# Kernel optimization log

Measured on AMD Instinct MI355X. Metric: run time of the kernel, lower is better.

## Reference

```python
import jax, jax.numpy as jnp
import numpy as np

NUM_HEADS = 12
HEAD_DIM = 64  # qkv_dim // num_heads = 768 // 12


def setup_inputs() -> dict:
    key = jax.random.key(0)
    ks = jax.random.split(key, 5)
    B, S, Dm = 4, 2048, 768
    x = jax.random.normal(ks[0], (B, S, Dm), dtype=jnp.float32)
    q_mask = jnp.ones((B, S), dtype=jnp.float32)
    sc = 1.0 / np.sqrt(Dm)
    Wq = jax.random.normal(ks[1], (Dm, Dm), dtype=jnp.float32) * sc
    Wk = jax.random.normal(ks[2], (Dm, Dm), dtype=jnp.float32) * sc
    Wv = jax.random.normal(ks[3], (Dm, Dm), dtype=jnp.float32) * sc
    Wo = jax.random.normal(ks[4], (Dm, Dm), dtype=jnp.float32) * sc
    return {"x": x, "q_mask": q_mask, "Wq": Wq, "Wk": Wk, "Wv": Wv, "Wo": Wo}


def _split_heads(t):
    # [b, s, qkv] -> [b, h, s, d]
    b, s, _ = t.shape
    return t.reshape(b, s, NUM_HEADS, HEAD_DIM).transpose(0, 2, 1, 3)


def reference(x, q_mask, Wq, Wk, Wv, Wo):
    # TAttention.forward with k=v=None -> self-attention, k_mask = q_mask.
    q = _split_heads(x @ Wq) * (1.0 / jnp.sqrt(jnp.asarray(HEAD_DIM, x.dtype)))
    k = _split_heads(x @ Wk)
    v = _split_heads(x @ Wv)
    logits_raw = jnp.einsum('bhqd,bhkd->bhqk', q, k)
    # additive mask: mask = outer(q_mask, k_mask) broadcast over heads
    mask = jnp.einsum('bq,bk->bqk', q_mask, q_mask)[:, None]  # [b,1,q,k]
    logits = logits_raw + (-100000.0) * (1.0 - mask)
    att = jax.nn.softmax(logits, axis=-1)  # dropout_rate=0 -> identity
    out = jnp.einsum('bhqk,bhkd->bhqd', att, v)
    b, h, s, d = out.shape
    out = out.transpose(0, 2, 1, 3).reshape(b, s, h * d)
    out = out @ Wo
    return (out, logits_raw)
```

## Files before the change

### kernel.cpp

```cpp
#include <hip/hip_runtime.h>

typedef _Float16 f16;
typedef __attribute__((ext_vector_type(4))) _Float16 f16x4;
typedef __attribute__((ext_vector_type(8))) _Float16 f16x8;
typedef __attribute__((ext_vector_type(4))) float f32x4;

#define NB 4
#define SS 2048
#define DM 768
#define NH 12
#define HDIM 64
#define NBH 48
#define MROWS 8192

#define XH_OFF   0ull
#define WT_OFF   12582912ull
#define QH_OFF   17301504ull
#define KH_OFF   29884416ull
#define VH_OFF   42467328ull
#define VT_OFF   55050240ull
#define AO_OFF   67633152ull

__device__ __forceinline__ void async_copy16(const void* g, void* l) {
  __builtin_amdgcn_global_load_lds((const __attribute__((address_space(1))) void*)g,
                                   (__attribute__((address_space(3))) void*)l, 16, 0, 0);
}

__global__ void k_cvt_x(const float* __restrict__ x, f16* __restrict__ xh, int n4) {
  int i = blockIdx.x * 256 + threadIdx.x;
  if (i >= n4) return;
  float4 v = ((const float4*)x)[i];
  f16x4 o;
  o.x = (f16)v.x; o.y = (f16)v.y; o.z = (f16)v.z; o.w = (f16)v.w;
  ((f16x4*)xh)[i] = o;
}

__global__ void k_wt(const float* __restrict__ Wq, const float* __restrict__ Wk,
                     const float* __restrict__ Wv, const float* __restrict__ Wo,
                     f16* __restrict__ wt) {
  __shared__ float t[32][33];
  const int w = blockIdx.z;
  const float* W = (w == 0) ? Wq : (w == 1) ? Wk : (w == 2) ? Wv : Wo;
  const int bx = blockIdx.x * 32, by = blockIdx.y * 32;
  const int tx = threadIdx.x, ty = threadIdx.y;
  t[ty][tx] = W[(size_t)(by + ty) * DM + bx + tx];
  __syncthreads();
  wt[(size_t)w * DM * DM + (size_t)(bx + ty) * DM + by + tx] = (f16)t[tx][ty];
}

template<int MODE>
__global__ __launch_bounds__(256) void k_gemm(const f16* __restrict__ A,
                                              const f16* __restrict__ Wt,
                                              float* __restrict__ outF,
                                              f16* __restrict__ Qh,
                                              f16* __restrict__ Kh,
                                              f16* __restrict__ Vh) {
  __shared__ f16 Al[128 * 32];
  __shared__ f16 Bl[128 * 32];
  const int tid = threadIdx.x, lane = tid & 63, wid = tid >> 6;
  const int mt = blockIdx.x;
  int w, ntile;
  if (MODE == 0) { w = blockIdx.y / 6; ntile = blockIdx.y % 6; }
  else           { w = 3;              ntile = blockIdx.y; }
  const f16* Wb = Wt + (size_t)w * DM * DM;

  f32x4 acc[4][4] = {};
  const int wr = (wid >> 1) * 64, wc = (wid & 1) * 64;

  const int r0 = tid >> 2, c8 = (tid & 3) * 8;
  const f16* As0 = A  + (size_t)(mt * 128 + r0) * DM + c8;
  const f16* As1 = A  + (size_t)(mt * 128 + r0 + 64) * DM + c8;
  const f16* Bs0 = Wb + (size_t)(ntile * 128 + r0) * DM + c8;
  const f16* Bs1 = Wb + (size_t)(ntile * 128 + r0 + 64) * DM + c8;
  f16* Ald0 = &Al[wid * 512];          f16* Ald1 = &Al[2048 + wid * 512];
  f16* Bld0 = &Bl[wid * 512];          f16* Bld1 = &Bl[2048 + wid * 512];

  for (int k0 = 0; k0 < DM; k0 += 32) {
    __syncthreads();
    async_copy16(As0 + k0, Ald0);
    async_copy16(As1 + k0, Ald1);
    async_copy16(Bs0 + k0, Bld0);
    async_copy16(Bs1 + k0, Bld1);
    __syncthreads();
    f16x8 af[4], bfr[4];
#pragma unroll
    for (int r = 0; r < 4; ++r)
      af[r] = *(const f16x8*)&Al[(wr + r * 16 + (lane & 15)) * 32 + (lane >> 4) * 8];
#pragma unroll
    for (int c = 0; c < 4; ++c)
      bfr[c] = *(const f16x8*)&Bl[(wc + c * 16 + (lane & 15)) * 32 + (lane >> 4) * 8];
#pragma unroll
    for (int r = 0; r < 4; ++r)
#pragma unroll
      for (int c = 0; c < 4; ++c)
        acc[r][c] = __builtin_amdgcn_mfma_f32_16x16x32_f16(af[r], bfr[c], acc[r][c], 0, 0, 0);
  }

#pragma unroll
  for (int r = 0; r < 4; ++r)
#pragma unroll
    for (int c = 0; c < 4; ++c)
#pragma unroll
      for (int i = 0; i < 4; ++i) {
        const int gm = mt * 128 + wr + r * 16 + (lane >> 4) * 4 + i;
        const int gn = ntile * 128 + wc + c * 16 + (lane & 15);
        const float v = acc[r][c][i];
        if (MODE == 1) {
          outF[(size_t)gm * DM + gn] = v;
        } else {
          const int b = gm >> 11, s = gm & 2047;
          const int h = gn >> 6, d = gn & 63;
          const size_t idx = ((size_t)(b * NH + h) * SS + s) * HDIM + d;
          if (w == 0)      Qh[idx] = (f16)(v * 0.125f);
          else if (w == 1) Kh[idx] = (f16)v;
          else             Vh[idx] = (f16)v;
        }
      }
}

__global__ void k_vt(const f16* __restrict__ Vh, f16* __restrict__ Vt) {
  const int lane = threadIdx.x & 63, wid = threadIdx.x >> 6;
  const int s = blockIdx.x * 64 + lane;
  const int bh = blockIdx.y;
#pragma unroll
  for (int p = 0; p < 2; ++p) {
    const int d0 = wid * 16 + p * 8;
    f16x8 v = *(const f16x8*)&Vh[((size_t)bh * SS + s) * HDIM + d0];
#pragma unroll
    for (int q = 0; q < 8; ++q)
      Vt[((size_t)bh * HDIM + d0 + q) * SS + s] = v[q];
  }
}

__global__ __launch_bounds__(256) void k_attn(const f16* __restrict__ Qh,
                                              const f16* __restrict__ Kh,
                                              const f16* __restrict__ Vt,
                                              const float* __restrict__ qm,
                                              float* __restrict__ logits,
                                              f16* __restrict__ AO) {
  __shared__ f16 Kl[64 * 64];
  __shared__ f16 Vl[64 * 64];
  __shared__ f16 Pl[4][16 * 72];
  const int tid = threadIdx.x, lane = tid & 63, wid = tid >> 6;
  const int qt = blockIdx.x, bh = blockIdx.y;
  const int b = bh / NH, h = bh - b * NH;
  const int q0 = qt * 128 + wid * 32;

  f16x8 qf[2][2];
#pragma unroll
  for (int rt = 0; rt < 2; ++rt)
#pragma unroll
    for (int ks = 0; ks < 2; ++ks)
      qf[rt][ks] = *(const f16x8*)&Qh[((size_t)bh * SS + q0 + rt * 16 + (lane & 15)) * HDIM +
                                      ks * 32 + (lane >> 4) * 8];

  float qmq[2][4];
#pragma unroll
  for (int rt = 0; rt < 2; ++rt)
#pragma unroll
    for (int i = 0; i < 4; ++i)
      qmq[rt][i] = qm[b * SS + q0 + rt * 16 + (lane >> 4) * 4 + i];

  float mrun[2][4], lrun[2][4];
#pragma unroll
  for (int rt = 0; rt < 2; ++rt)
#pragma unroll
    for (int i = 0; i < 4; ++i) { mrun[rt][i] = -3.0e38f; lrun[rt][i] = 0.f; }
  f32x4 o[2][4] = {};

  float* const logbase = logits + (size_t)bh * SS * SS;
  const char* const Kbase = (const char*)Kh + (size_t)bh * SS * HDIM * 2;
  const char* const Vbase = (const char*)Vt + (size_t)bh * HDIM * SS * 2;
  const int r0s = tid >> 3;
  const int wb0 = (tid & 7) * 16;

  for (int c = 0; c < 32; ++c) {
    __syncthreads();
#pragma unroll
    for (int j = 0; j < 2; ++j) {
      const int r = r0s + j * 32;
      const int swb = wb0 ^ ((r & 7) << 4);
      async_copy16(Kbase + (size_t)(c * 64 + r) * 128 + swb,
                   (char*)Kl + wid * 1024 + j * 4096);
      async_copy16(Vbase + (size_t)r * 4096 + c * 128 + swb,
                   (char*)Vl + wid * 1024 + j * 4096);
    }
    __syncthreads();

    f16x8 kf[4][2], vf[4][2];
#pragma unroll
    for (int t = 0; t < 4; ++t)
#pragma unroll
      for (int ks = 0; ks < 2; ++ks) {
        const int row = t * 16 + (lane & 15);
        const int byt = row * 128 + ((ks * 64 + (lane >> 4) * 16) ^ ((row & 7) << 4));
        kf[t][ks] = *(const f16x8*)((const char*)Kl + byt);
        vf[t][ks] = *(const f16x8*)((const char*)Vl + byt);
      }

    f32x4 sacc[2][4];
#pragma unroll
    for (int rt = 0; rt < 2; ++rt)
#pragma unroll
      for (int ct = 0; ct < 4; ++ct) {
        f32x4 z = {};
        z = __builtin_amdgcn_mfma_f32_16x16x32_f16(qf[rt][0], kf[ct][0], z, 0, 0, 0);
        sacc[rt][ct] = __builtin_amdgcn_mfma_f32_16x16x32_f16(qf[rt][1], kf[ct][1], z, 0, 0, 0);
      }

#pragma unroll
    for (int rt = 0; rt < 2; ++rt)
#pragma unroll
      for (int ct = 0; ct < 4; ++ct)
#pragma unroll
        for (int i = 0; i < 4; ++i) {
          const int gq = q0 + rt * 16 + (lane >> 4) * 4 + i;
          const int gk = c * 64 + ct * 16 + (lane & 15);
          logbase[(size_t)gq * SS + gk] = sacc[rt][ct][i];
        }

    float qmk[4];
#pragma unroll
    for (int ct = 0; ct < 4; ++ct) qmk[ct] = qm[b * SS + c * 64 + ct * 16 + (lane & 15)];

#pragma unroll
    for (int rt = 0; rt < 2; ++rt) {
      float p[4][4];
      float pm[4] = {-3.0e38f, -3.0e38f, -3.0e38f, -3.0e38f};
#pragma unroll
      for (int ct = 0; ct < 4; ++ct)
#pragma unroll
        for (int i = 0; i < 4; ++i) {
          const float sb = sacc[rt][ct][i] - 100000.f * (1.f - qmq[rt][i] * qmk[ct]);
          p[ct][i] = sb;
          pm[i] = fmaxf(pm[i], sb);
        }
#pragma unroll
      for (int off = 1; off < 16; off <<= 1)
#pragma unroll
        for (int i = 0; i < 4; ++i) pm[i] = fmaxf(pm[i], __shfl_xor(pm[i], off));

      float scal[4];
#pragma unroll
      for (int i = 0; i < 4; ++i) {
        const float mnew = fmaxf(mrun[rt][i], pm[i]);
        scal[i] = __expf(mrun[rt][i] - mnew);
        mrun[rt][i] = mnew;
      }
#pragma unroll
      for (int ct = 0; ct < 4; ++ct)
#pragma unroll
        for (int i = 0; i < 4; ++i) p[ct][i] = __expf(p[ct][i] - mrun[rt][i]);

      float rs[4];
#pragma unroll
      for (int i = 0; i < 4; ++i) rs[i] = p[0][i] + p[1][i] + p[2][i] + p[3][i];
#pragma unroll
      for (int off = 1; off < 16; off <<= 1)
#pragma unroll
        for (int i = 0; i < 4; ++i) rs[i] += __shfl_xor(rs[i], off);
#pragma unroll
      for (int i = 0; i < 4; ++i) lrun[rt][i] = lrun[rt][i] * scal[i] + rs[i];
#pragma unroll
      for (int dt = 0; dt < 4; ++dt)
#pragma unroll
        for (int i = 0; i < 4; ++i) o[rt][dt][i] *= scal[i];

      f16* pw = Pl[wid];
#pragma unroll
      for (int ct = 0; ct < 4; ++ct)
#pragma unroll
        for (int i = 0; i < 4; ++i)
          pw[((lane >> 4) * 4 + i) * 72 + ct * 16 + (lane & 15)] = (f16)p[ct][i];
      asm volatile("s_waitcnt lgkmcnt(0)" ::: "memory");
      const f16x8 pf0 = *(const f16x8*)&pw[(lane & 15) * 72 + (lane >> 4) * 8];
      const f16x8 pf1 = *(const f16x8*)&pw[(lane & 15) * 72 + 32 + (lane >> 4) * 8];
#pragma unroll
      for (int dt = 0; dt < 4; ++dt) {
        o[rt][dt] = __builtin_amdgcn_mfma_f32_16x16x32_f16(pf0, vf[dt][0], o[rt][dt], 0, 0, 0);
        o[rt][dt] = __builtin_amdgcn_mfma_f32_16x16x32_f16(pf1, vf[dt][1], o[rt][dt], 0, 0, 0);
      }
    }
  }

#pragma unroll
  for (int rt = 0; rt < 2; ++rt)
#pragma unroll
    for (int i = 0; i < 4; ++i) {
      const float inv = 1.0f / lrun[rt][i];
      const int gq = q0 + rt * 16 + (lane >> 4) * 4 + i;
#pragma unroll
      for (int dt = 0; dt < 4; ++dt)
        AO[((size_t)b * SS + gq) * DM + h * HDIM + dt * 16 + (lane & 15)] =
            (f16)(o[rt][dt][i] * inv);
    }
}

extern "C" void kernel_launch(void* const* d_in, const int* in_sizes, int n_in,
                              void* d_out, int out_size, void* d_ws, size_t ws_size,
                              hipStream_t stream) {
  const float* x  = (const float*)d_in[0];
  const float* qm = (const float*)d_in[1];
  const float* Wq = (const float*)d_in[2];
  const float* Wk = (const float*)d_in[3];
  const float* Wv = (const float*)d_in[4];
  const float* Wo = (const float*)d_in[5];
  float* out    = (float*)d_out;
  float* logits = out + 6291456;

  char* ws = (char*)d_ws;
  f16* xh = (f16*)(ws + XH_OFF);
  f16* wt = (f16*)(ws + WT_OFF);
  f16* qh = (f16*)(ws + QH_OFF);
  f16* kh = (f16*)(ws + KH_OFF);
  f16* vh = (f16*)(ws + VH_OFF);
  f16* vt = (f16*)(ws + VT_OFF);
  f16* ao = (f16*)(ws + AO_OFF);

  const int n4 = MROWS * DM / 4;
  k_cvt_x<<<(n4 + 255) / 256, 256, 0, stream>>>(x, xh, n4);
  k_wt<<<dim3(24, 24, 4), dim3(32, 32), 0, stream>>>(Wq, Wk, Wv, Wo, wt);
  k_gemm<0><<<dim3(64, 18), 256, 0, stream>>>(xh, wt, nullptr, qh, kh, vh);
  k_vt<<<dim3(32, 48), 256, 0, stream>>>(vh, vt);
  k_attn<<<dim3(16, 48), 256, 0, stream>>>(qh, kh, vt, qm, logits, ao);
  k_gemm<1><<<dim3(64, 6), 256, 0, stream>>>(ao, wt, out, nullptr, nullptr, nullptr);
}
```

Baseline: 1.057 ms.

## Double-buffer LDS tiles and transpose MFMA operands for vectorized logits stores

Both the projection GEMM and the attention kernel now double-buffer their LDS tiles, prefetching the next K/V or A/B slice while the current one is computed, which removes one barrier per iteration. The attention kernel swaps the MFMA operand order so each lane holds four consecutive key columns of one query row. That lets the fp32 logits be written as 16-byte nontemporal stores, reduces the row-softmax reductions to two shuffles, and makes the P and output stores vectorized. Wave priority is raised around the MFMA blocks, and the trade-off is twice the LDS footprint, which may lower occupancy.

```diff
diff --git a/kernel.cpp b/kernel.cpp
--- a/kernel.cpp
+++ b/kernel.cpp
@@ -10,7 +10,6 @@
 #define DM 768
 #define NH 12
 #define HDIM 64
-#define NBH 48
 #define MROWS 8192
 
 #define XH_OFF   0ull
@@ -55,8 +54,8 @@
                                               f16* __restrict__ Qh,
                                               f16* __restrict__ Kh,
                                               f16* __restrict__ Vh) {
-  __shared__ f16 Al[128 * 32];
-  __shared__ f16 Bl[128 * 32];
+  __shared__ f16 Al[2][128 * 32];
+  __shared__ f16 Bl[2][128 * 32];
   const int tid = threadIdx.x, lane = tid & 63, wid = tid >> 6;
   const int mt = blockIdx.x;
   int w, ntile;
@@ -72,28 +71,34 @@
   const f16* As1 = A  + (size_t)(mt * 128 + r0 + 64) * DM + c8;
   const f16* Bs0 = Wb + (size_t)(ntile * 128 + r0) * DM + c8;
   const f16* Bs1 = Wb + (size_t)(ntile * 128 + r0 + 64) * DM + c8;
-  f16* Ald0 = &Al[wid * 512];          f16* Ald1 = &Al[2048 + wid * 512];
-  f16* Bld0 = &Bl[wid * 512];          f16* Bld1 = &Bl[2048 + wid * 512];
-
-  for (int k0 = 0; k0 < DM; k0 += 32) {
+
+  auto stage = [&](int bi, int k0) {
+    async_copy16(As0 + k0, &Al[bi][wid * 512]);
+    async_copy16(As1 + k0, &Al[bi][2048 + wid * 512]);
+    async_copy16(Bs0 + k0, &Bl[bi][wid * 512]);
+    async_copy16(Bs1 + k0, &Bl[bi][2048 + wid * 512]);
+  };
+
+  stage(0, 0);
+  for (int k0 = 0, it = 0; k0 < DM; k0 += 32, ++it) {
+    const int cur = it & 1;
+    asm volatile("s_waitcnt vmcnt(0)" ::: "memory");
     __syncthreads();
-    async_copy16(As0 + k0, Ald0);
-    async_copy16(As1 + k0, Ald1);
-    async_copy16(Bs0 + k0, Bld0);
-    async_copy16(Bs1 + k0, Bld1);
-    __syncthreads();
+    if (k0 + 32 < DM) stage(cur ^ 1, k0 + 32);
     f16x8 af[4], bfr[4];
 #pragma unroll
     for (int r = 0; r < 4; ++r)
-      af[r] = *(const f16x8*)&Al[(wr + r * 16 + (lane & 15)) * 32 + (lane >> 4) * 8];
+      af[r] = *(const f16x8*)&Al[cur][(wr + r * 16 + (lane & 15)) * 32 + (lane >> 4) * 8];
 #pragma unroll
     for (int c = 0; c < 4; ++c)
-      bfr[c] = *(const f16x8*)&Bl[(wc + c * 16 + (lane & 15)) * 32 + (lane >> 4) * 8];
+      bfr[c] = *(const f16x8*)&Bl[cur][(wc + c * 16 + (lane & 15)) * 32 + (lane >> 4) * 8];
+    __builtin_amdgcn_s_setprio(1);
 #pragma unroll
     for (int r = 0; r < 4; ++r)
 #pragma unroll
       for (int c = 0; c < 4; ++c)
         acc[r][c] = __builtin_amdgcn_mfma_f32_16x16x32_f16(af[r], bfr[c], acc[r][c], 0, 0, 0);
+    __builtin_amdgcn_s_setprio(0);
   }
 
 #pragma unroll
@@ -138,9 +143,9 @@
                                               const float* __restrict__ qm,
                                               float* __restrict__ logits,
                                               f16* __restrict__ AO) {
-  __shared__ f16 Kl[64 * 64];
-  __shared__ f16 Vl[64 * 64];
-  __shared__ f16 Pl[4][16 * 72];
+  __shared__ f16 Kl[2][64 * 64];
+  __shared__ f16 Vl[2][64 * 64];
+  __shared__ f16 Pl[4][16 * 76];
   const int tid = threadIdx.x, lane = tid & 63, wid = tid >> 6;
   const int qt = blockIdx.x, bh = blockIdx.y;
   const int b = bh / NH, h = bh - b * NH;
@@ -154,18 +159,12 @@
       qf[rt][ks] = *(const f16x8*)&Qh[((size_t)bh * SS + q0 + rt * 16 + (lane & 15)) * HDIM +
                                       ks * 32 + (lane >> 4) * 8];
 
-  float qmq[2][4];
+  float qmq[2];
 #pragma unroll
   for (int rt = 0; rt < 2; ++rt)
-#pragma unroll
-    for (int i = 0; i < 4; ++i)
-      qmq[rt][i] = qm[b * SS + q0 + rt * 16 + (lane >> 4) * 4 + i];
-
-  float mrun[2][4], lrun[2][4];
-#pragma unroll
-  for (int rt = 0; rt < 2; ++rt)
-#pragma unroll
-    for (int i = 0; i < 4; ++i) { mrun[rt][i] = -3.0e38f; lrun[rt][i] = 0.f; }
+    qmq[rt] = qm[b * SS + q0 + rt * 16 + (lane & 15)];
+
+  float mrun[2] = {-3.0e38f, -3.0e38f}, lrun[2] = {0.f, 0.f};
   f32x4 o[2][4] = {};
 
   float* const logbase = logits + (size_t)bh * SS * SS;
@@ -174,18 +173,24 @@
   const int r0s = tid >> 3;
   const int wb0 = (tid & 7) * 16;
 
-  for (int c = 0; c < 32; ++c) {
-    __syncthreads();
+  auto STAGE = [&](int bi, int c) {
 #pragma unroll
     for (int j = 0; j < 2; ++j) {
       const int r = r0s + j * 32;
       const int swb = wb0 ^ ((r & 7) << 4);
       async_copy16(Kbase + (size_t)(c * 64 + r) * 128 + swb,
-                   (char*)Kl + wid * 1024 + j * 4096);
+                   (char*)&Kl[bi][0] + wid * 1024 + j * 4096);
       async_copy16(Vbase + (size_t)r * 4096 + c * 128 + swb,
-                   (char*)Vl + wid * 1024 + j * 4096);
+                   (char*)&Vl[bi][0] + wid * 1024 + j * 4096);
     }
+  };
+
+  STAGE(0, 0);
+  for (int c = 0; c < 32; ++c) {
+    const int cur = c & 1;
+    asm volatile("s_waitcnt vmcnt(0)" ::: "memory");
     __syncthreads();
+    if (c + 1 < 32) STAGE(cur ^ 1, c + 1);
 
     f16x8 kf[4][2], vf[4][2];
 #pragma unroll
@@ -194,106 +199,101 @@
       for (int ks = 0; ks < 2; ++ks) {
         const int row = t * 16 + (lane & 15);
         const int byt = row * 128 + ((ks * 64 + (lane >> 4) * 16) ^ ((row & 7) << 4));
-        kf[t][ks] = *(const f16x8*)((const char*)Kl + byt);
-        vf[t][ks] = *(const f16x8*)((const char*)Vl + byt);
-      }
+        kf[t][ks] = *(const f16x8*)((const char*)&Kl[cur][0] + byt);
+        vf[t][ks] = *(const f16x8*)((const char*)&Vl[cur][0] + byt);
+      }
+
+    float4 qmk4[4];
+#pragma unroll
+    for (int ct = 0; ct < 4; ++ct)
+      qmk4[ct] = *(const float4*)&qm[b * SS + c * 64 + ct * 16 + (lane >> 4) * 4];
 
     f32x4 sacc[2][4];
+    __builtin_amdgcn_s_setprio(1);
 #pragma unroll
     for (int rt = 0; rt < 2; ++rt)
 #pragma unroll
       for (int ct = 0; ct < 4; ++ct) {
         f32x4 z = {};
-        z = __builtin_amdgcn_mfma_f32_16x16x32_f16(qf[rt][0], kf[ct][0], z, 0, 0, 0);
-        sacc[rt][ct] = __builtin_amdgcn_mfma_f32_16x16x32_f16(qf[rt][1], kf[ct][1], z, 0, 0, 0);
-      }
+        z = __builtin_amdgcn_mfma_f32_16x16x32_f16(kf[ct][0], qf[rt][0], z, 0, 0, 0);
+        sacc[rt][ct] = __builtin_amdgcn_mfma_f32_16x16x32_f16(kf[ct][1], qf[rt][1], z, 0, 0, 0);
+      }
+    __builtin_amdgcn_s_setprio(0);
 
 #pragma unroll
     for (int rt = 0; rt < 2; ++rt)
 #pragma unroll
-      for (int ct = 0; ct < 4; ++ct)
-#pragma unroll
-        for (int i = 0; i < 4; ++i) {
-          const int gq = q0 + rt * 16 + (lane >> 4) * 4 + i;
-          const int gk = c * 64 + ct * 16 + (lane & 15);
-          logbase[(size_t)gq * SS + gk] = sacc[rt][ct][i];
-        }
-
-    float qmk[4];
-#pragma unroll
-    for (int ct = 0; ct < 4; ++ct) qmk[ct] = qm[b * SS + c * 64 + ct * 16 + (lane & 15)];
+      for (int ct = 0; ct < 4; ++ct) {
+        const int gq = q0 + rt * 16 + (lane & 15);
+        const int gk = c * 64 + ct * 16 + (lane >> 4) * 4;
+        __builtin_nontemporal_store(sacc[rt][ct], (f32x4*)(logbase + (size_t)gq * SS + gk));
+      }
 
 #pragma unroll
     for (int rt = 0; rt < 2; ++rt) {
       float p[4][4];
-      float pm[4] = {-3.0e38f, -3.0e38f, -3.0e38f, -3.0e38f};
+      float pm = -3.0e38f;
 #pragma unroll
       for (int ct = 0; ct < 4; ++ct)
 #pragma unroll
         for (int i = 0; i < 4; ++i) {
-          const float sb = sacc[rt][ct][i] - 100000.f * (1.f - qmq[rt][i] * qmk[ct]);
-          p[ct][i] = sb;
-          pm[i] = fmaxf(pm[i], sb);
+          p[ct][i] = sacc[rt][ct][i] + (qmq[rt] * ((const float*)&qmk4[ct])[i] - 1.f) * 100000.f;
+          pm = fmaxf(pm, p[ct][i]);
         }
-#pragma unroll
-      for (int off = 1; off < 16; off <<= 1)
-#pragma unroll
-        for (int i = 0; i < 4; ++i) pm[i] = fmaxf(pm[i], __shfl_xor(pm[i], off));
-
-      float scal[4];
-#pragma unroll
-      for (int i = 0; i < 4; ++i) {
-        const float mnew = fmaxf(mrun[rt][i], pm[i]);
-        scal[i] = __expf(mrun[rt][i] - mnew);
-        mrun[rt][i] = mnew;
-      }
+      pm = fmaxf(pm, __shfl_xor(pm, 16));
+      pm = fmaxf(pm, __shfl_xor(pm, 32));
+      const float mnew = fmaxf(mrun[rt], pm);
+      const float scal = __expf(mrun[rt] - mnew);
+      mrun[rt] = mnew;
+      float rs = 0.f;
 #pragma unroll
       for (int ct = 0; ct < 4; ++ct)
 #pragma unroll
-        for (int i = 0; i < 4; ++i) p[ct][i] = __expf(p[ct][i] - mrun[rt][i]);
-
-      float rs[4];
-#pragma unroll
-      for (int i = 0; i < 4; ++i) rs[i] = p[0][i] + p[1][i] + p[2][i] + p[3][i];
-#pragma unroll
-      for (int off = 1; off < 16; off <<= 1)
-#pragma unroll
-        for (int i = 0; i < 4; ++i) rs[i] += __shfl_xor(rs[i], off);
-#pragma unroll
-      for (int i = 0; i < 4; ++i) lrun[rt][i] = lrun[rt][i] * scal[i] + rs[i];
+        for (int i = 0; i < 4; ++i) {
+          p[ct][i] = __expf(p[ct][i] - mnew);
+          rs += p[ct][i];
+        }
+      rs += __shfl_xor(rs, 16);
+      rs += __shfl_xor(rs, 32);
+      lrun[rt] = lrun[rt] * scal + rs;
 #pragma unroll
       for (int dt = 0; dt < 4; ++dt)
 #pragma unroll
-        for (int i = 0; i < 4; ++i) o[rt][dt][i] *= scal[i];
+        for (int i = 0; i < 4; ++i) o[rt][dt][i] *= scal;
 
       f16* pw = Pl[wid];
 #pragma unroll
-      for (int ct = 0; ct < 4; ++ct)
-#pragma unroll
-        for (int i = 0; i < 4; ++i)
-          pw[((lane >> 4) * 4 + i) * 72 + ct * 16 + (lane & 15)] = (f16)p[ct][i];
+      for (int ct = 0; ct < 4; ++ct) {
+        f16x4 pk;
+#pragma unroll
+        for (int i = 0; i < 4; ++i) pk[i] = (f16)p[ct][i];
+        *(f16x4*)&pw[(lane & 15) * 76 + ct * 16 + (lane >> 4) * 4] = pk;
+      }
       asm volatile("s_waitcnt lgkmcnt(0)" ::: "memory");
-      const f16x8 pf0 = *(const f16x8*)&pw[(lane & 15) * 72 + (lane >> 4) * 8];
-      const f16x8 pf1 = *(const f16x8*)&pw[(lane & 15) * 72 + 32 + (lane >> 4) * 8];
+      const f16x8 pf0 = *(const f16x8*)&pw[(lane & 15) * 76 + (lane >> 4) * 8];
+      const f16x8 pf1 = *(const f16x8*)&pw[(lane & 15) * 76 + 32 + (lane >> 4) * 8];
+      __builtin_amdgcn_s_setprio(1);
 #pragma unroll
       for (int dt = 0; dt < 4; ++dt) {
-        o[rt][dt] = __builtin_amdgcn_mfma_f32_16x16x32_f16(pf0, vf[dt][0], o[rt][dt], 0, 0, 0);
-        o[rt][dt] = __builtin_amdgcn_mfma_f32_16x16x32_f16(pf1, vf[dt][1], o[rt][dt], 0, 0, 0);
-      }
+        o[rt][dt] = __builtin_amdgcn_mfma_f32_16x16x32_f16(vf[dt][0], pf0, o[rt][dt], 0, 0, 0);
+        o[rt][dt] = __builtin_amdgcn_mfma_f32_16x16x32_f16(vf[dt][1], pf1, o[rt][dt], 0, 0, 0);
+      }
+      __builtin_amdgcn_s_setprio(0);
     }
   }
 
 #pragma unroll
-  for (int rt = 0; rt < 2; ++rt)
-#pragma unroll
-    for (int i = 0; i < 4; ++i) {
-      const float inv = 1.0f / lrun[rt][i];
-      const int gq = q0 + rt * 16 + (lane >> 4) * 4 + i;
-#pragma unroll
-      for (int dt = 0; dt < 4; ++dt)
-        AO[((size_t)b * SS + gq) * DM + h * HDIM + dt * 16 + (lane & 15)] =
-            (f16)(o[rt][dt][i] * inv);
+  for (int rt = 0; rt < 2; ++rt) {
+    const float inv = 1.0f / lrun[rt];
+    const int gq = q0 + rt * 16 + (lane & 15);
+#pragma unroll
+    for (int dt = 0; dt < 4; ++dt) {
+      f16x4 ov;
+#pragma unroll
+      for (int i = 0; i < 4; ++i) ov[i] = (f16)(o[rt][dt][i] * inv);
+      *(f16x4*)&AO[((size_t)b * SS + gq) * DM + h * HDIM + dt * 16 + (lane >> 4) * 4] = ov;
     }
+  }
 }
 
 extern "C" void kernel_launch(void* const* d_in, const int* in_sizes, int n_in,
@@ -301,10 +301,6 @@
                               hipStream_t stream) {
   const float* x  = (const float*)d_in[0];
   const float* qm = (const float*)d_in[1];
-  const float* Wq = (const float*)d_in[2];
-  const float* Wk = (const float*)d_in[3];
-  const float* Wv = (const float*)d_in[4];
-  const float* Wo = (const float*)d_in[5];
   float* out    = (float*)d_out;
   float* logits = out + 6291456;
 
@@ -319,7 +315,8 @@
 
   const int n4 = MROWS * DM / 4;
   k_cvt_x<<<(n4 + 255) / 256, 256, 0, stream>>>(x, xh, n4);
-  k_wt<<<dim3(24, 24, 4), dim3(32, 32), 0, stream>>>(Wq, Wk, Wv, Wo, wt);
+  k_wt<<<dim3(24, 24, 4), dim3(32, 32), 0, stream>>>((const float*)d_in[2], (const float*)d_in[3],
+                                                     (const float*)d_in[4], (const float*)d_in[5], wt);
   k_gemm<0><<<dim3(64, 18), 256, 0, stream>>>(xh, wt, nullptr, qh, kh, vh);
   k_vt<<<dim3(32, 48), 256, 0, stream>>>(vh, vt);
   k_attn<<<dim3(16, 48), 256, 0, stream>>>(qh, kh, vt, qm, logits, ao);
```

New measurement: 1.071 ms. Within noise of the previous version (+1.3%).
